# Kernel optimization log

Measured on AMD Instinct MI355X. Metric: run time of the kernel, lower is better.

Reference implementation:

```python
import jax, jax.numpy as jnp
import numpy as np
from jax import lax

B, L, D = 4, 4096, 1024
K = 4          # kernel_size
E = 2          # expand_dim
C = D * E      # expanded channels


def setup_inputs() -> dict:
    key = jax.random.key(0)
    ks = jax.random.split(key, 6)
    s_in = 1.0 / np.sqrt(D)
    s_ex = 1.0 / np.sqrt(C)
    s_cv = 1.0 / np.sqrt(K)  # torch Conv1d init: 1/sqrt(in_ch/groups * k) = 1/sqrt(k) for depthwise
    return {
        "x": jax.random.normal(ks[0], (B, L, D), dtype=jnp.float32),
        "W_exp": jax.random.uniform(ks[1], (D, C), jnp.float32, -s_in, s_in),
        "b_exp": jax.random.uniform(ks[2], (C,), jnp.float32, -s_in, s_in),
        "conv_w": jax.random.uniform(ks[3], (K, 1, C), jnp.float32, -s_cv, s_cv),  # LIO layout
        "conv_b": jax.random.uniform(ks[4], (C,), jnp.float32, -s_cv, s_cv),
        "W_cmp": jax.random.uniform(ks[5], (C, D), jnp.float32, -s_ex, s_ex),
        "b_cmp": jax.random.uniform(jax.random.fold_in(key, 7), (D,), jnp.float32, -s_ex, s_ex),
    }


def reference(x, W_exp, b_exp, conv_w, conv_b, W_cmp, b_cmp):
    # expand: (b,l,d) -> (b,l,C)
    xe = x @ W_exp + b_exp
    # depthwise causal conv over length: left-pad K-1 (equivalent to torch
    # padding=K-1 on both sides followed by [..., :l] slice)
    y = lax.conv_general_dilated(
        xe, conv_w,
        window_strides=(1,),
        padding=[(K - 1, 0)],
        dimension_numbers=("NLC", "LIO", "NLC"),
        feature_group_count=C,
    ) + conv_b
    # compress: (b,l,C) -> (b,l,d)
    return y @ W_cmp + b_cmp
```

## Files before the change

kernel.cpp:

```cpp
#include <hip/hip_runtime.h>
#include <stdint.h>

#define B_ 4
#define L_ 4096
#define D_ 1024
#define C_ 2048
#define M_ (B_ * L_)
#define LCH 16

typedef __attribute__((ext_vector_type(8))) short s16x8;
typedef __attribute__((ext_vector_type(4))) float fx4;
typedef unsigned short bfu;

__device__ __forceinline__ float bits2f(short s) {
  return __uint_as_float(((uint32_t)(unsigned short)s) << 16);
}
__device__ __forceinline__ bfu f2bf(float f) {
  uint32_t u = __float_as_uint(f);
  uint32_t r = (u + 0x7FFFu + ((u >> 16) & 1u)) >> 16;
  return (bfu)r;
}

__device__ __forceinline__ void gload_lds16(const void* g, void* l) {
  __builtin_amdgcn_global_load_lds(
      (const __attribute__((address_space(1))) void*)g,
      (__attribute__((address_space(3))) void*)l, 16, 0, 0);
}

#define BAR() asm volatile("s_barrier" ::: "memory")
#define LGKM0() asm volatile("s_waitcnt lgkmcnt(0)" ::: "memory")
#define VMW8() asm volatile("s_waitcnt vmcnt(8)" ::: "memory")
#define VMW4() asm volatile("s_waitcnt vmcnt(4)" ::: "memory")
#define VMW0() asm volatile("s_waitcnt vmcnt(0)" ::: "memory")

__global__ __launch_bounds__(256) void cvt_f32_bf16(const float* __restrict__ in,
                                                    bfu* __restrict__ out, int n8) {
  const int stride = gridDim.x * blockDim.x;
  for (int i = blockIdx.x * blockDim.x + threadIdx.x; i < n8; i += stride) {
    const size_t off = (size_t)i * 8;
    fx4 a = *(const fx4*)(in + off);
    fx4 b = *(const fx4*)(in + off + 4);
    s16x8 o;
#pragma unroll
    for (int j = 0; j < 4; j++) {
      o[j] = (short)f2bf(a[j]);
      o[j + 4] = (short)f2bf(b[j]);
    }
    *reinterpret_cast<s16x8*>(out + off) = o;
  }
}

template <int R, int CC>
__global__ __launch_bounds__(256) void transpose_cvt(const float* __restrict__ in,
                                                     bfu* __restrict__ out) {
  __shared__ float tile[32][33];
  const int bx = blockIdx.x, by = blockIdx.y, tx = threadIdx.x;
  for (int j = threadIdx.y; j < 32; j += 8)
    tile[j][tx] = in[(size_t)(by * 32 + j) * CC + bx * 32 + tx];
  __syncthreads();
  for (int j = threadIdx.y; j < 32; j += 8)
    out[(size_t)(bx * 32 + j) * R + by * 32 + tx] = f2bf(tile[tx][j]);
}


template <int KD>
__device__ __forceinline__ void stage_half(const bfu* __restrict__ Mt, int r0, int kb,
                                           bfu* region, int t) {
#pragma unroll
  for (int h = 0; h < 2; h++) {
    const int u = t + h * 512;
    const int srow = u >> 2;
    const int sslot = (u & 3) ^ ((srow >> 1) & 3);
    gload_lds16(Mt + (size_t)(r0 + srow) * KD + kb + sslot * 8, region + u * 8);
  }
}

#define LF(bytoff) \
  (*reinterpret_cast<const s16x8*>(reinterpret_cast<const char*>(lds) + (bytoff)))

template <int MM, int N, int KD, bool OUT_BF16>
__global__ __launch_bounds__(512, 2) void gemm256(const bfu* __restrict__ A,
                                                  const bfu* __restrict__ Bt,
                                                  const float* __restrict__ bias,
                                                  void* __restrict__ Cptr) {
  __shared__ bfu lds[2 * 4 * 8192];
  const int t = threadIdx.x;
  const int lane = t & 63, wid = t >> 6;
  const int wr = wid >> 2, wc = wid & 3;
  const int lr = lane & 15, lg = lane >> 4;
  const int cpx = gridDim.x >> 3;
  const int li = (blockIdx.x & 7) * cpx + (blockIdx.x >> 3);
  const int row0 = (li % (MM / 256)) * 256;
  const int col0 = (li / (MM / 256)) * 256;
  constexpr int ntk = KD / 64;
  const int abase = ((wr * 128 + lr) * 64 + lg * 16) ^ (((lr >> 1) & 3) << 4);
  const int bbase = ((wc * 64 + lr) * 64 + lg * 16) ^ (((lr >> 1) & 3) << 4);

  fx4 acc[8][4] = {};

  stage_half<KD>(A, row0, 0, lds + 0, t);
  stage_half<KD>(Bt, col0, 0, lds + 16384, t);
  stage_half<KD>(A, row0, 32, lds + 8192, t);
  stage_half<KD>(Bt, col0, 32, lds + 24576, t);
  stage_half<KD>(A, row0, 64, lds + 32768 + 0, t);
  stage_half<KD>(Bt, col0, 64, lds + 32768 + 16384, t);
  VMW8();
  BAR();

  for (int tau = 0; tau < ntk; ++tau) {
    const int cbb = (tau & 1) ? 65536 : 0;
    bfu* nb_ = (tau & 1) ? lds : lds + 32768;
    s16x8 af[4], bf4[4];

#pragma unroll
    for (int m = 0; m < 4; m++) af[m] = LF(cbb + abase + m * 1024);
#pragma unroll
    for (int n = 0; n < 4; n++) bf4[n] = LF(cbb + 32768 + bbase + n * 1024);
    if (tau + 1 < ntk) stage_half<KD>(A, row0, (tau + 1) * 64 + 32, nb_ + 8192, t);
    BAR();
    LGKM0();
    __builtin_amdgcn_s_setprio(1);
#pragma unroll
    for (int m = 0; m < 4; m++)
#pragma unroll
      for (int n = 0; n < 4; n++)
        acc[m][n] = __builtin_amdgcn_mfma_f32_16x16x32_bf16(af[m], bf4[n], acc[m][n], 0, 0, 0);
    __builtin_amdgcn_s_setprio(0);
    BAR();

#pragma unroll
    for (int m = 0; m < 4; m++) af[m] = LF(cbb + abase + 4096 + m * 1024);
    if (tau + 1 < ntk) stage_half<KD>(Bt, col0, (tau + 1) * 64 + 32, nb_ + 24576, t);
    BAR();
    LGKM0();
    __builtin_amdgcn_s_setprio(1);
#pragma unroll
    for (int m = 0; m < 4; m++)
#pragma unroll
      for (int n = 0; n < 4; n++)
        acc[m + 4][n] = __builtin_amdgcn_mfma_f32_16x16x32_bf16(af[m], bf4[n], acc[m + 4][n], 0, 0, 0);
    __builtin_amdgcn_s_setprio(0);
    if (tau < ntk - 1) VMW8();
    else VMW0();
    BAR();

#pragma unroll
    for (int m = 0; m < 4; m++) af[m] = LF(cbb + 16384 + abase + m * 1024);
#pragma unroll
    for (int n = 0; n < 4; n++) bf4[n] = LF(cbb + 49152 + bbase + n * 1024);
    if (tau + 2 < ntk) stage_half<KD>(A, row0, (tau + 2) * 64, lds + (cbb >> 1), t);
    BAR();
    LGKM0();
    __builtin_amdgcn_s_setprio(1);
#pragma unroll
    for (int m = 0; m < 4; m++)
#pragma unroll
      for (int n = 0; n < 4; n++)
        acc[m][n] = __builtin_amdgcn_mfma_f32_16x16x32_bf16(af[m], bf4[n], acc[m][n], 0, 0, 0);
    __builtin_amdgcn_s_setprio(0);
    BAR();

#pragma unroll
    for (int m = 0; m < 4; m++) af[m] = LF(cbb + 16384 + abase + 4096 + m * 1024);
    if (tau + 2 < ntk) stage_half<KD>(Bt, col0, (tau + 2) * 64, lds + (cbb >> 1) + 16384, t);
    BAR();
    LGKM0();
    __builtin_amdgcn_s_setprio(1);
#pragma unroll
    for (int m = 0; m < 4; m++)
#pragma unroll
      for (int n = 0; n < 4; n++)
        acc[m + 4][n] = __builtin_amdgcn_mfma_f32_16x16x32_bf16(af[m], bf4[n], acc[m + 4][n], 0, 0, 0);
    __builtin_amdgcn_s_setprio(0);
    if (tau < ntk - 2) VMW8();
    else if (tau == ntk - 2) VMW4();
    BAR();
  }

  float bv[4];
#pragma unroll
  for (int n = 0; n < 4; n++) bv[n] = bias[col0 + wc * 64 + n * 16 + lr];
#pragma unroll
  for (int m = 0; m < 8; m++)
#pragma unroll
    for (int n = 0; n < 4; n++)
#pragma unroll
      for (int r = 0; r < 4; r++) {
        const int row = row0 + wr * 128 + m * 16 + lg * 4 + r;
        const int col = col0 + wc * 64 + n * 16 + lr;
        const float v = acc[m][n][r] + bv[n];
        if constexpr (OUT_BF16)
          ((bfu*)Cptr)[(size_t)row * N + col] = f2bf(v);
        else
          ((float*)Cptr)[(size_t)row * N + col] = v;
      }
}

__global__ __launch_bounds__(256) void dwconv_slide(const bfu* __restrict__ xe,
                                                    const float* __restrict__ cw,
                                                    const float* __restrict__ cb,
                                                    bfu* __restrict__ y) {
  const int nchunk = L_ / LCH;
  const int b = blockIdx.x / nchunk;
  const int l0 = (blockIdx.x % nchunk) * LCH;
  const int cg = threadIdx.x << 3;

  float w[4][8], bias8[8];
#pragma unroll
  for (int tt = 0; tt < 4; tt++) {
    fx4 w0 = *(const fx4*)(cw + tt * C_ + cg);
    fx4 w1 = *(const fx4*)(cw + tt * C_ + cg + 4);
#pragma unroll
    for (int i = 0; i < 4; i++) {
      w[tt][i] = w0[i];
      w[tt][i + 4] = w1[i];
    }
  }
  {
    fx4 c0 = *(const fx4*)(cb + cg), c1 = *(const fx4*)(cb + cg + 4);
#pragma unroll
    for (int i = 0; i < 4; i++) {
      bias8[i] = c0[i];
      bias8[i + 4] = c1[i];
    }
  }

  const size_t base = ((size_t)b * L_ + l0) * C_ + cg;
  s16x8 h0 = {}, h1 = {}, h2 = {};
  if (l0 != 0) {
    h0 = *reinterpret_cast<const s16x8*>(xe + base - 3 * C_);
    h1 = *reinterpret_cast<const s16x8*>(xe + base - 2 * C_);
    h2 = *reinterpret_cast<const s16x8*>(xe + base - 1 * C_);
  }
#pragma unroll
  for (int i = 0; i < LCH; i++) {
    s16x8 h3 = *reinterpret_cast<const s16x8*>(xe + base + (size_t)i * C_);
    s16x8 o;
#pragma unroll
    for (int j = 0; j < 8; j++) {
      float v = bias8[j];
      v = fmaf(bits2f(h0[j]), w[0][j], v);
      v = fmaf(bits2f(h1[j]), w[1][j], v);
      v = fmaf(bits2f(h2[j]), w[2][j], v);
      v = fmaf(bits2f(h3[j]), w[3][j], v);
      o[j] = (short)f2bf(v);
    }
    *reinterpret_cast<s16x8*>(y + base + (size_t)i * C_) = o;
    h0 = h1;
    h1 = h2;
    h2 = h3;
  }
}

extern "C" void kernel_launch(void* const* d_in, const int* in_sizes, int n_in,
                              void* d_out, int out_size, void* d_ws, size_t ws_size,
                              hipStream_t stream) {
  const float* x = (const float*)d_in[0];
  const float* W_exp = (const float*)d_in[1];
  const float* b_exp = (const float*)d_in[2];
  const float* cw = (const float*)d_in[3];
  const float* cb = (const float*)d_in[4];
  const float* W_cmp = (const float*)d_in[5];
  const float* b_cmp = (const float*)d_in[6];
  float* out = (float*)d_out;

  char* ws = (char*)d_ws;
  bfu* wexp_t = (bfu*)(ws);
  bfu* wcmp_t = (bfu*)(ws + (4u << 20));
  bfu* xb = (bfu*)(ws + (8u << 20));
  bfu* xe = (bfu*)(ws + (40u << 20));
  bfu* y = (bfu*)(ws + (104u << 20));

  cvt_f32_bf16<<<2048, 256, 0, stream>>>(x, xb, M_ * D_ / 8);
  transpose_cvt<D_, C_><<<dim3(C_ / 32, D_ / 32), dim3(32, 8), 0, stream>>>(W_exp, wexp_t);
  transpose_cvt<C_, D_><<<dim3(D_ / 32, C_ / 32), dim3(32, 8), 0, stream>>>(W_cmp, wcmp_t);
  gemm256<M_, C_, D_, true><<<512, 512, 0, stream>>>(xb, wexp_t, b_exp, xe);
  dwconv_slide<<<B_ * (L_ / LCH), 256, 0, stream>>>(xe, cw, cb, y);
  gemm256<M_, D_, C_, false><<<256, 512, 0, stream>>>(y, wcmp_t, b_cmp, out);
}
```

Measured before the change: 201.0 us.

## Fuse depthwise causal conv into compress GEMM A-tile staging

```diff
diff --git a/kernel.cpp b/kernel.cpp
--- a/kernel.cpp
+++ b/kernel.cpp
@@ -6,10 +6,10 @@
 #define D_ 1024
 #define C_ 2048
 #define M_ (B_ * L_)
-#define LCH 16
 
 typedef __attribute__((ext_vector_type(8))) short s16x8;
 typedef __attribute__((ext_vector_type(4))) float fx4;
+typedef __attribute__((ext_vector_type(4))) unsigned int ux4;
 typedef unsigned short bfu;
 
 __device__ __forceinline__ float bits2f(short s) {
@@ -29,6 +29,7 @@
 
 #define BAR() asm volatile("s_barrier" ::: "memory")
 #define LGKM0() asm volatile("s_waitcnt lgkmcnt(0)" ::: "memory")
+#define VMW23() asm volatile("s_waitcnt vmcnt(23)" ::: "memory")
 #define VMW8() asm volatile("s_waitcnt vmcnt(8)" ::: "memory")
 #define VMW4() asm volatile("s_waitcnt vmcnt(4)" ::: "memory")
 #define VMW0() asm volatile("s_waitcnt vmcnt(0)" ::: "memory")
@@ -60,6 +61,17 @@
   __syncthreads();
   for (int j = threadIdx.y; j < 32; j += 8)
     out[(size_t)(bx * 32 + j) * R + by * 32 + tx] = f2bf(tile[tx][j]);
+}
+
+__global__ __launch_bounds__(256) void prep_cw(const float* __restrict__ cw,
+                                               const float* __restrict__ cb,
+                                               uint32_t* __restrict__ wtab) {
+  const int c = blockIdx.x * 256 + threadIdx.x;
+  uint32_t* o = wtab + c * 8;
+#pragma unroll
+  for (int t4 = 0; t4 < 4; t4++)
+    o[t4] = ((uint32_t)f2bf(cw[t4 * C_ + 2 * c + 1]) << 16) | f2bf(cw[t4 * C_ + 2 * c]);
+  o[4] = ((uint32_t)f2bf(cb[2 * c + 1]) << 16) | f2bf(cb[2 * c]);
 }
 
 
@@ -196,60 +208,179 @@
       }
 }
 
-__global__ __launch_bounds__(256) void dwconv_slide(const bfu* __restrict__ xe,
-                                                    const float* __restrict__ cw,
-                                                    const float* __restrict__ cb,
-                                                    bfu* __restrict__ y) {
-  const int nchunk = L_ / LCH;
-  const int b = blockIdx.x / nchunk;
-  const int l0 = (blockIdx.x % nchunk) * LCH;
-  const int cg = threadIdx.x << 3;
-
-  float w[4][8], bias8[8];
-#pragma unroll
-  for (int tt = 0; tt < 4; tt++) {
-    fx4 w0 = *(const fx4*)(cw + tt * C_ + cg);
-    fx4 w1 = *(const fx4*)(cw + tt * C_ + cg + 4);
-#pragma unroll
-    for (int i = 0; i < 4; i++) {
-      w[tt][i] = w0[i];
-      w[tt][i + 4] = w1[i];
+struct Batch {
+  uint32_t x[19];
+  ux4 w;
+  uint32_t cb;
+};
+
+__device__ __forceinline__ void batch_load(Batch& b, const bfu* __restrict__ xe,
+                                           const uint32_t* __restrict__ wtab,
+                                           int row0, int rg, int cp, int tile) {
+  const bfu* p = xe + (size_t)(row0 + rg * 16 - 3) * C_ + tile * 64 + cp * 2;
+#pragma unroll
+  for (int j = 0; j < 19; j++)
+    b.x[j] = *reinterpret_cast<const uint32_t*>(p + (size_t)j * C_);
+  const uint32_t* wp = wtab + (tile * 32 + cp) * 8;
+  b.w = *reinterpret_cast<const ux4*>(wp);
+  b.cb = wp[4];
+}
+
+__device__ __forceinline__ void conv_write(bfu* nbase, const Batch& b, int rg, int cp,
+                                           bool zero_head) {
+  bfu* region = nbase + ((cp & 16) ? 8192 : 0);
+  char* vrow = reinterpret_cast<char*>(region) + rg * 1024;
+  const int colb = (cp & 15) * 4;
+  float wl[4], wh[4];
+#pragma unroll
+  for (int t4 = 0; t4 < 4; t4++) {
+    const uint32_t wv = b.w[t4];
+    wl[t4] = bits2f((short)(wv & 0xffffu));
+    wh[t4] = bits2f((short)(wv >> 16));
+  }
+  const float cbl = bits2f((short)(b.cb & 0xffffu));
+  const float cbh = bits2f((short)(b.cb >> 16));
+  uint32_t xx[19];
+#pragma unroll
+  for (int j = 0; j < 19; j++) xx[j] = b.x[j];
+  if (zero_head && rg == 0) {
+    xx[0] = 0;
+    xx[1] = 0;
+    xx[2] = 0;
+  }
+#pragma unroll
+  for (int j = 0; j < 16; j++) {
+    float lo = cbl, hi = cbh;
+#pragma unroll
+    for (int t4 = 0; t4 < 4; t4++) {
+      const uint32_t v = xx[j + t4];
+      lo = fmaf(bits2f((short)(v & 0xffffu)), wl[t4], lo);
+      hi = fmaf(bits2f((short)(v >> 16)), wh[t4], hi);
     }
-  }
-  {
-    fx4 c0 = *(const fx4*)(cb + cg), c1 = *(const fx4*)(cb + cg + 4);
-#pragma unroll
-    for (int i = 0; i < 4; i++) {
-      bias8[i] = c0[i];
-      bias8[i + 4] = c1[i];
+    const uint32_t o = ((uint32_t)f2bf(hi) << 16) | f2bf(lo);
+    *reinterpret_cast<uint32_t*>(vrow + j * 64 + (colb ^ (((j >> 1) & 3) << 4))) = o;
+  }
+}
+
+template <int MM, int N, int KD>
+__global__ __launch_bounds__(512, 2) void gemm256_conv(
+    const bfu* __restrict__ xe, const bfu* __restrict__ Bt,
+    const uint32_t* __restrict__ wtab, const float* __restrict__ bias,
+    float* __restrict__ Cptr) {
+  __shared__ bfu lds[2 * 4 * 8192];
+  const int t = threadIdx.x;
+  const int lane = t & 63, wid = t >> 6;
+  const int wr = wid >> 2, wc = wid & 3;
+  const int lr = lane & 15, lg = lane >> 4;
+  const int cpx = gridDim.x >> 3;
+  const int li = (blockIdx.x & 7) * cpx + (blockIdx.x >> 3);
+  const int row0 = (li % (MM / 256)) * 256;
+  const int col0 = (li / (MM / 256)) * 256;
+  constexpr int ntk = KD / 64;
+  const int abase = ((wr * 128 + lr) * 64 + lg * 16) ^ (((lr >> 1) & 3) << 4);
+  const int bbase = ((wc * 64 + lr) * 64 + lg * 16) ^ (((lr >> 1) & 3) << 4);
+  const int rg = lane >> 2;
+  const int cp = wid * 4 + (lane & 3);
+  const bool zh = (row0 & (L_ - 1)) == 0;
+
+  fx4 acc[8][4] = {};
+  Batch bt;
+
+  batch_load(bt, xe, wtab, row0, rg, cp, 0);
+  stage_half<KD>(Bt, col0, 0, lds + 16384, t);
+  stage_half<KD>(Bt, col0, 32, lds + 24576, t);
+  stage_half<KD>(Bt, col0, 64, lds + 32768 + 16384, t);
+  conv_write(lds, bt, rg, cp, zh);
+  batch_load(bt, xe, wtab, row0, rg, cp, 1);
+  VMW23();
+  LGKM0();
+  BAR();
+
+  for (int tau = 0; tau < ntk; ++tau) {
+    const int cbb = (tau & 1) ? 65536 : 0;
+    bfu* nb_ = (tau & 1) ? lds : lds + 32768;
+    s16x8 af[4], bf4[4];
+
+#pragma unroll
+    for (int m = 0; m < 4; m++) af[m] = LF(cbb + abase + m * 1024);
+#pragma unroll
+    for (int n = 0; n < 4; n++) bf4[n] = LF(cbb + 32768 + bbase + n * 1024);
+    BAR();
+    LGKM0();
+    __builtin_amdgcn_s_setprio(1);
+#pragma unroll
+    for (int m = 0; m < 4; m++)
+#pragma unroll
+      for (int n = 0; n < 4; n++)
+        acc[m][n] = __builtin_amdgcn_mfma_f32_16x16x32_bf16(af[m], bf4[n], acc[m][n], 0, 0, 0);
+    __builtin_amdgcn_s_setprio(0);
+    BAR();
+
+#pragma unroll
+    for (int m = 0; m < 4; m++) af[m] = LF(cbb + abase + 4096 + m * 1024);
+    if (tau + 1 < ntk) stage_half<KD>(Bt, col0, (tau + 1) * 64 + 32, nb_ + 24576, t);
+    BAR();
+    LGKM0();
+    __builtin_amdgcn_s_setprio(1);
+#pragma unroll
+    for (int m = 0; m < 4; m++)
+#pragma unroll
+      for (int n = 0; n < 4; n++)
+        acc[m + 4][n] = __builtin_amdgcn_mfma_f32_16x16x32_bf16(af[m], bf4[n], acc[m + 4][n], 0, 0, 0);
+    __builtin_amdgcn_s_setprio(0);
+    BAR();
+
+#pragma unroll
+    for (int m = 0; m < 4; m++) af[m] = LF(cbb + 16384 + abase + m * 1024);
+#pragma unroll
+    for (int n = 0; n < 4; n++) bf4[n] = LF(cbb + 49152 + bbase + n * 1024);
+    BAR();
+    if (wid < 4 && tau + 1 < ntk) conv_write(nb_, bt, rg, cp, zh);
+    LGKM0();
+    __builtin_amdgcn_s_setprio(1);
+#pragma unroll
+    for (int m = 0; m < 4; m++)
+#pragma unroll
+      for (int n = 0; n < 4; n++)
+        acc[m][n] = __builtin_amdgcn_mfma_f32_16x16x32_bf16(af[m], bf4[n], acc[m][n], 0, 0, 0);
+    __builtin_amdgcn_s_setprio(0);
+    BAR();
+
+#pragma unroll
+    for (int m = 0; m < 4; m++) af[m] = LF(cbb + 16384 + abase + 4096 + m * 1024);
+    if (tau + 2 < ntk) stage_half<KD>(Bt, col0, (tau + 2) * 64, lds + (cbb >> 1) + 16384, t);
+    BAR();
+    if (wid >= 4 && tau + 1 < ntk) conv_write(nb_, bt, rg, cp, zh);
+    LGKM0();
+    __builtin_amdgcn_s_setprio(1);
+#pragma unroll
+    for (int m = 0; m < 4; m++)
+#pragma unroll
+      for (int n = 0; n < 4; n++)
+        acc[m + 4][n] = __builtin_amdgcn_mfma_f32_16x16x32_bf16(af[m], bf4[n], acc[m + 4][n], 0, 0, 0);
+    __builtin_amdgcn_s_setprio(0);
+    if (tau + 2 < ntk) {
+      batch_load(bt, xe, wtab, row0, rg, cp, tau + 2);
+      VMW23();
+    } else {
+      VMW0();
     }
-  }
-
-  const size_t base = ((size_t)b * L_ + l0) * C_ + cg;
-  s16x8 h0 = {}, h1 = {}, h2 = {};
-  if (l0 != 0) {
-    h0 = *reinterpret_cast<const s16x8*>(xe + base - 3 * C_);
-    h1 = *reinterpret_cast<const s16x8*>(xe + base - 2 * C_);
-    h2 = *reinterpret_cast<const s16x8*>(xe + base - 1 * C_);
-  }
-#pragma unroll
-  for (int i = 0; i < LCH; i++) {
-    s16x8 h3 = *reinterpret_cast<const s16x8*>(xe + base + (size_t)i * C_);
-    s16x8 o;
-#pragma unroll
-    for (int j = 0; j < 8; j++) {
-      float v = bias8[j];
-      v = fmaf(bits2f(h0[j]), w[0][j], v);
-      v = fmaf(bits2f(h1[j]), w[1][j], v);
-      v = fmaf(bits2f(h2[j]), w[2][j], v);
-      v = fmaf(bits2f(h3[j]), w[3][j], v);
-      o[j] = (short)f2bf(v);
-    }
-    *reinterpret_cast<s16x8*>(y + base + (size_t)i * C_) = o;
-    h0 = h1;
-    h1 = h2;
-    h2 = h3;
-  }
+    BAR();
+  }
+
+  float bv[4];
+#pragma unroll
+  for (int n = 0; n < 4; n++) bv[n] = bias[col0 + wc * 64 + n * 16 + lr];
+#pragma unroll
+  for (int m = 0; m < 8; m++)
+#pragma unroll
+    for (int n = 0; n < 4; n++)
+#pragma unroll
+      for (int r = 0; r < 4; r++) {
+        const int row = row0 + wr * 128 + m * 16 + lg * 4 + r;
+        const int col = col0 + wc * 64 + n * 16 + lr;
+        Cptr[(size_t)row * N + col] = acc[m][n][r] + bv[n];
+      }
 }
 
 extern "C" void kernel_launch(void* const* d_in, const int* in_sizes, int n_in,
@@ -269,12 +400,12 @@
   bfu* wcmp_t = (bfu*)(ws + (4u << 20));
   bfu* xb = (bfu*)(ws + (8u << 20));
   bfu* xe = (bfu*)(ws + (40u << 20));
-  bfu* y = (bfu*)(ws + (104u << 20));
+  uint32_t* wtab = (uint32_t*)(ws + (104u << 20));
 
   cvt_f32_bf16<<<2048, 256, 0, stream>>>(x, xb, M_ * D_ / 8);
   transpose_cvt<D_, C_><<<dim3(C_ / 32, D_ / 32), dim3(32, 8), 0, stream>>>(W_exp, wexp_t);
   transpose_cvt<C_, D_><<<dim3(D_ / 32, C_ / 32), dim3(32, 8), 0, stream>>>(W_cmp, wcmp_t);
+  prep_cw<<<4, 256, 0, stream>>>(cw, cb, wtab);
   gemm256<M_, C_, D_, true><<<512, 512, 0, stream>>>(xb, wexp_t, b_exp, xe);
-  dwconv_slide<<<B_ * (L_ / LCH), 256, 0, stream>>>(xe, cw, cb, y);
-  gemm256<M_, D_, C_, false><<<256, 512, 0, stream>>>(y, wcmp_t, b_cmp, out);
-}
+  gemm256_conv<M_, D_, C_><<<256, 512, 0, stream>>>(xe, wcmp_t, wtab, b_cmp, out);
+}
```

New measurement: 260.0 us. +29.4%, slower.
